# Kernel optimization log

Measured on AMD Instinct MI355X. Metric: run time of the kernel, lower is better.

Reference implementation:

```python
import jax, jax.numpy as jnp
import numpy as np

H = 16          # num_attention_heads
HD = 64         # attention_head_size
ALPHA = 1.5
BANDWIDTH = 1.0
A_EXP = 0.5     # sinkhorn-like exponent 'a'
DIST_SCALE = float(HD)  # alpha < 2 => scale by head_size
EPS = 1e-12     # F.normalize eps


def setup_inputs() -> dict:
    key = jax.random.key(0)
    ks = jax.random.split(key, 5)
    B, L, D = 2, 1024, 1024
    w_scale = 0.02  # keep distances in a non-degenerate range for the power-law kernel
    x = jax.random.normal(ks[0], (B, L, D), dtype=jnp.float32)
    WQ = jax.random.normal(ks[1], (D, D), dtype=jnp.float32) * w_scale
    WK = jax.random.normal(ks[2], (D, D), dtype=jnp.float32) * w_scale
    WV = jax.random.normal(ks[3], (D, D), dtype=jnp.float32) * w_scale
    WO = jax.random.normal(ks[4], (D, D), dtype=jnp.float32) * w_scale
    z = jnp.zeros((D,), dtype=jnp.float32)
    return {"x": x, "WQ": WQ, "bQ": z, "WK": WK, "bK": z,
            "WV": WV, "bV": z, "WO": WO, "bO": z}


def _heads(t, B, L):
    # [B, L, H*HD] -> [B, H, L, HD]
    return t.reshape(B, L, H, HD).transpose(0, 2, 1, 3)


def reference(x, WQ, bQ, WK, bK, WV, bV, WO, bO):
    B, L, D = x.shape
    q = _heads(x @ WQ + bQ, B, L)   # [B,H,L,HD]
    k = _heads(x @ WK + bK, B, L)
    v = _heads(x @ WV + bV, B, L)

    # torch.cdist(q, k, p=2): pairwise euclidean distance [B,H,L,L]
    q2 = jnp.sum(q * q, axis=-1)                      # [B,H,L]
    k2 = jnp.sum(k * k, axis=-1)                      # [B,H,L]
    qk = jnp.einsum('bhid,bhjd->bhij', q, k)          # [B,H,L,L]
    d2 = q2[..., :, None] + k2[..., None, :] - 2.0 * qk
    g_dist = jnp.sqrt(jnp.maximum(d2, EPS)) / DIST_SCALE

    # alpha < 2: power-law kernel (1 + g/sqrt(bw))^(-(d_intrinsic + alpha))
    attn_score = (1.0 + g_dist / np.sqrt(BANDWIDTH)) ** (-(HD + ALPHA))

    # a > 0: Sinkhorn-style row/col renormalization
    N_R = jnp.sum(attn_score, axis=-1)                # [B,H,L] row sums
    N_C = jnp.sum(attn_score, axis=-2)                # [B,H,L] col sums
    K_tilde = (N_R ** (-A_EXP))[..., :, None] * attn_score * (N_C ** (-A_EXP))[..., None, :]

    # F.normalize(p=1, dim=3); entries are positive so |.| sum == sum
    attention_probs = K_tilde / jnp.maximum(jnp.sum(K_tilde, axis=-1, keepdims=True), EPS)

    out = jnp.einsum('bhij,bhjd->bhid', attention_probs, v)   # [B,H,L,HD]
    out = out.transpose(0, 2, 1, 3).reshape(B, L, H * HD)
    return out @ WO + bO
```

## Files before the change

kernel.cpp:

```cpp
#include <hip/hip_runtime.h>
#include <math.h>


typedef __attribute__((ext_vector_type(8))) short short8;
typedef __attribute__((ext_vector_type(4))) float f32x4;

__device__ inline unsigned short f2bf(float f) {
  unsigned int u = __float_as_uint(f);
  unsigned int r = (u + 0x7FFFu + ((u >> 16) & 1u)) >> 16;
  return (unsigned short)r;
}
__device__ inline float bf2f(unsigned short s) {
  return __uint_as_float(((unsigned int)s) << 16);
}
__device__ inline float score_fn(float dot, float sq) {
  float d2 = fmaxf(fmaf(-2.f, dot, sq), 1e-12f);
  float sd = __builtin_amdgcn_sqrtf(d2);
  float lg = __builtin_amdgcn_logf(fmaf(sd, 0.015625f, 1.0f));
  return __builtin_amdgcn_exp2f(-65.5f * lg);
}
__device__ inline unsigned int cvtpk(float lo, float hi) {
  unsigned int r;
  asm("v_cvt_pk_bf16_f32 %0, %1, %2" : "=v"(r) : "v"(lo), "v"(hi));
  return r;
}
#define GLD16(lptr, gptr)                                                      \
  __builtin_amdgcn_global_load_lds(                                            \
      (const __attribute__((address_space(1))) void*)(gptr),                   \
      (__attribute__((address_space(3))) void*)(lptr), 16, 0, 0)
#define MEMFENCE() asm volatile("" ::: "memory")
#define HARD_BARRIER()                 \
  do {                                 \
    __builtin_amdgcn_s_barrier();      \
    MEMFENCE();                        \
  } while (0)

__global__ __launch_bounds__(256) void prep(const float* __restrict__ x,
                                            unsigned short* __restrict__ xb,
                                            const float* __restrict__ W0,
                                            const float* __restrict__ W1,
                                            const float* __restrict__ W2,
                                            const float* __restrict__ W3,
                                            unsigned short* __restrict__ T0,
                                            unsigned short* __restrict__ T1,
                                            unsigned short* __restrict__ T2,
                                            unsigned short* __restrict__ T3) {
  __shared__ float T[32][33];
  int bx = blockIdx.x;
  if (bx < 2048) {
    int i = bx * 256 + threadIdx.x;
    float4 v = ((const float4*)x)[i];
    xb[4 * i + 0] = f2bf(v.x);
    xb[4 * i + 1] = f2bf(v.y);
    xb[4 * i + 2] = f2bf(v.z);
    xb[4 * i + 3] = f2bf(v.w);
    return;
  }
  int idx = bx - 2048;
  int z = idx >> 10, rem = idx & 1023;
  const float* W = z == 0 ? W0 : z == 1 ? W1 : z == 2 ? W2 : W3;
  unsigned short* WT = z == 0 ? T0 : z == 1 ? T1 : z == 2 ? T2 : T3;
  int k0 = (rem >> 5) * 32, n0 = (rem & 31) * 32;
  int c = threadIdx.x & 31, r8 = threadIdx.x >> 5;
#pragma unroll
  for (int it = 0; it < 4; ++it) {
    int rr = r8 + it * 8;
    T[rr][c] = W[(size_t)(k0 + rr) * 1024 + n0 + c];
  }
  __syncthreads();
#pragma unroll
  for (int it = 0; it < 4; ++it) {
    int rr = r8 + it * 8;
    WT[(size_t)(n0 + rr) * 1024 + k0 + c] = f2bf(T[c][rr]);
  }
}

__global__ __launch_bounds__(256, 3) void gemm_qkv(const unsigned short* __restrict__ A,
                                                   const unsigned short* __restrict__ B0,
                                                   const unsigned short* __restrict__ B1,
                                                   const unsigned short* __restrict__ B2,
                                                   const float* __restrict__ c0,
                                                   const float* __restrict__ c1,
                                                   const float* __restrict__ c2,
                                                   void* __restrict__ Y0,
                                                   void* __restrict__ Y1,
                                                   void* __restrict__ Y2,
                                                   float* __restrict__ sq0,
                                                   float* __restrict__ sq1,
                                                   float* __restrict__ sq2,
                                                   int m0, int m1, int m2) {
  int z = blockIdx.z;
  const unsigned short* BT = z == 0 ? B0 : z == 1 ? B1 : B2;
  const float* bias = z == 0 ? c0 : z == 1 ? c1 : c2;
  void* Y = z == 0 ? Y0 : z == 1 ? Y1 : Y2;
  float* sq = z == 0 ? sq0 : z == 1 ? sq1 : sq2;
  int mode = z == 0 ? m0 : z == 1 ? m1 : m2;

  __shared__ __align__(16) unsigned short As[2][128 * 32];
  __shared__ __align__(16) unsigned short Bs[2][64 * 32];
  int tid = threadIdx.x;
  int w = tid >> 6, l = tid & 63, g = l >> 4, l15 = l & 15;
  int wm = w >> 1, wn = w & 1;
  int bm = blockIdx.x * 128, bn = blockIdx.y * 64;

  const int cA0 = tid, cA1 = tid + 256;
  const int rA0 = cA0 >> 2, sA0 = (cA0 & 3) ^ (rA0 & 3) ^ ((rA0 >> 2) & 3);
  const int rA1 = cA1 >> 2, sA1 = (cA1 & 3) ^ (rA1 & 3) ^ ((rA1 >> 2) & 3);
  const int rB0 = tid >> 2, sB0 = (tid & 3) ^ (rB0 & 3) ^ ((rB0 >> 2) & 3);

  GLD16(&As[0][cA0 * 8], &A[(size_t)(bm + rA0) * 1024 + sA0 * 8]);
  GLD16(&As[0][cA1 * 8], &A[(size_t)(bm + rA1) * 1024 + sA1 * 8]);
  GLD16(&Bs[0][tid * 8], &BT[(size_t)(bn + rB0) * 1024 + sB0 * 8]);

  f32x4 acc[4][2];
#pragma unroll
  for (int mi = 0; mi < 4; ++mi)
#pragma unroll
    for (int ni = 0; ni < 2; ++ni)
#pragma unroll
      for (int r = 0; r < 4; ++r) acc[mi][ni][r] = 0.f;

  int arow[4], aslot[4], brow[2], bslot[2];
#pragma unroll
  for (int mi = 0; mi < 4; ++mi) {
    arow[mi] = wm * 64 + mi * 16 + l15;
    aslot[mi] = g ^ (arow[mi] & 3) ^ ((arow[mi] >> 2) & 3);
  }
#pragma unroll
  for (int ni = 0; ni < 2; ++ni) {
    brow[ni] = wn * 32 + ni * 16 + l15;
    bslot[ni] = g ^ (brow[ni] & 3) ^ ((brow[ni] >> 2) & 3);
  }

  __syncthreads();
  for (int t = 0; t < 32; ++t) {
    int cur = t & 1;
    if (t < 31) {
      int kn = (t + 1) * 32;
      GLD16(&As[cur ^ 1][cA0 * 8], &A[(size_t)(bm + rA0) * 1024 + kn + sA0 * 8]);
      GLD16(&As[cur ^ 1][cA1 * 8], &A[(size_t)(bm + rA1) * 1024 + kn + sA1 * 8]);
      GLD16(&Bs[cur ^ 1][tid * 8], &BT[(size_t)(bn + rB0) * 1024 + kn + sB0 * 8]);
    }
    short8 a[4], b[2];
#pragma unroll
    for (int mi = 0; mi < 4; ++mi)
      a[mi] = *(const short8*)&As[cur][arow[mi] * 32 + aslot[mi] * 8];
#pragma unroll
    for (int ni = 0; ni < 2; ++ni)
      b[ni] = *(const short8*)&Bs[cur][brow[ni] * 32 + bslot[ni] * 8];
#pragma unroll
    for (int mi = 0; mi < 4; ++mi)
#pragma unroll
      for (int ni = 0; ni < 2; ++ni)
        acc[mi][ni] = __builtin_amdgcn_mfma_f32_16x16x32_bf16(a[mi], b[ni], acc[mi][ni], 0, 0, 0);
    __syncthreads();
  }

  float rowsq[4][4];
#pragma unroll
  for (int mi = 0; mi < 4; ++mi)
#pragma unroll
    for (int r = 0; r < 4; ++r) rowsq[mi][r] = 0.f;

#pragma unroll
  for (int ni = 0; ni < 2; ++ni) {
    int n = bn + wn * 32 + ni * 16 + l15;
    float bv = bias[n];
#pragma unroll
    for (int mi = 0; mi < 4; ++mi) {
#pragma unroll
      for (int r = 0; r < 4; ++r) {
        int m = bm + wm * 64 + mi * 16 + 4 * g + r;
        float v = acc[mi][ni][r] + bv;
        if (mode == 0) {
          int b = m >> 10, ll = m & 1023, h = n >> 6, hd = n & 63;
          unsigned short ush = f2bf(v);
          ((unsigned short*)Y)[(((size_t)(b * 16 + h) * 1024) + ll) * 64 + hd] = ush;
          float f = bf2f(ush);
          rowsq[mi][r] = fmaf(f, f, rowsq[mi][r]);
        } else if (mode == 1) {
          int b = m >> 10, ll = m & 1023, h = n >> 6, hd = n & 63;
          int jp = (ll & ~31) | (((ll >> 2) & 3) * 8 + ((ll >> 4) & 1) * 4 + (ll & 3));
          ((unsigned short*)Y)[(((size_t)(b * 16 + h) * 64) + hd) * 1024 + jp] = f2bf(v);
        } else {
          ((float*)Y)[(size_t)m * 1024 + n] = v;
        }
      }
    }
  }

  if (sq != nullptr) {
    float* Sq = (float*)&As[0][0];
#pragma unroll
    for (int mi = 0; mi < 4; ++mi)
#pragma unroll
      for (int r = 0; r < 4; ++r) {
        float s = rowsq[mi][r];
        s += __shfl_xor(s, 1);
        s += __shfl_xor(s, 2);
        s += __shfl_xor(s, 4);
        s += __shfl_xor(s, 8);
        rowsq[mi][r] = s;
      }
    if (l15 == 0) {
#pragma unroll
      for (int mi = 0; mi < 4; ++mi)
#pragma unroll
        for (int r = 0; r < 4; ++r)
          Sq[wn * 128 + wm * 64 + mi * 16 + 4 * g + r] = rowsq[mi][r];
    }
    __syncthreads();
    if (tid < 128) {
      float s = Sq[tid] + Sq[128 + tid];
      int m = bm + tid, b = m >> 10, ll = m & 1023;
      int h = bn >> 6;
      sq[(size_t)(b * 16 + h) * 1024 + ll] = s;
    }
  }
}

__global__ __launch_bounds__(256) void gemm_st(const unsigned short* __restrict__ A,
                                               const unsigned short* __restrict__ BT,
                                               const float* __restrict__ bias,
                                               float* __restrict__ Y) {
  __shared__ __align__(16) unsigned short As[2][64 * 64];
  __shared__ __align__(16) unsigned short Bs[2][64 * 64];
  int tid = threadIdx.x;
  int w = tid >> 6, l = tid & 63, g = l >> 4, l15 = l & 15;
  int bm = blockIdx.x * 64, bn = blockIdx.y * 64;
  const int arow = w * 16 + l15;
  const int x7 = l15 & 7;

  const int i0s = tid, i1s = 256 + tid;
  const int r0 = i0s >> 3, s0 = (i0s & 7) ^ (r0 & 7);
  const int r1 = i1s >> 3, s1 = (i1s & 7) ^ (r1 & 7);

  GLD16(&As[0][i0s * 8], &A[(size_t)(bm + r0) * 1024 + s0 * 8]);
  GLD16(&As[0][i1s * 8], &A[(size_t)(bm + r1) * 1024 + s1 * 8]);
  GLD16(&Bs[0][i0s * 8], &BT[(size_t)(bn + r0) * 1024 + s0 * 8]);
  GLD16(&Bs[0][i1s * 8], &BT[(size_t)(bn + r1) * 1024 + s1 * 8]);

  f32x4 acc[4];
#pragma unroll
  for (int t = 0; t < 4; ++t)
#pragma unroll
    for (int r = 0; r < 4; ++r) acc[t][r] = 0.f;

  __syncthreads();
  for (int t = 0; t < 16; ++t) {
    int cur = t & 1;
    if (t < 15) {
      int kn = (t + 1) * 64;
      GLD16(&As[cur ^ 1][i0s * 8], &A[(size_t)(bm + r0) * 1024 + kn + s0 * 8]);
      GLD16(&As[cur ^ 1][i1s * 8], &A[(size_t)(bm + r1) * 1024 + kn + s1 * 8]);
      GLD16(&Bs[cur ^ 1][i0s * 8], &BT[(size_t)(bn + r0) * 1024 + kn + s0 * 8]);
      GLD16(&Bs[cur ^ 1][i1s * 8], &BT[(size_t)(bn + r1) * 1024 + kn + s1 * 8]);
    }
#pragma unroll
    for (int kc = 0; kc < 2; ++kc) {
      short8 a = *(const short8*)&As[cur][arow * 64 + ((kc * 4 + g) ^ x7) * 8];
#pragma unroll
      for (int tt = 0; tt < 4; ++tt) {
        short8 b = *(const short8*)&Bs[cur][(tt * 16 + l15) * 64 + ((kc * 4 + g) ^ x7) * 8];
        acc[tt] = __builtin_amdgcn_mfma_f32_16x16x32_bf16(a, b, acc[tt], 0, 0, 0);
      }
    }
    __syncthreads();
  }

#pragma unroll
  for (int t = 0; t < 4; ++t) {
    int n = bn + 16 * t + l15;
    float bv = bias[n];
#pragma unroll
    for (int r = 0; r < 4; ++r) {
      int m = bm + w * 16 + 4 * g + r;
      Y[(size_t)m * 1024 + n] = acc[t][r] + bv;
    }
  }
}

__global__ __launch_bounds__(256, 4) void colsum_mfma(const unsigned short* __restrict__ Qb,
                                                      const unsigned short* __restrict__ Kb,
                                                      const float* __restrict__ q2,
                                                      const float* __restrict__ k2,
                                                      float* __restrict__ rnc) {
  __shared__ __align__(16) unsigned short Qd[3][64 * 64];
  __shared__ __align__(16) float q2s[1024];
  int bh = blockIdx.x, jt = blockIdx.y;
  int tid = threadIdx.x, w = tid >> 6, l = tid & 63;
  int g = l >> 4, l15 = l & 15;
  const int x7 = l15 & 7;
  const unsigned short* Qp = Qb + (size_t)bh * 65536;
  const unsigned short* Kp = Kb + (size_t)bh * 65536;
  int j = jt * 64 + w * 16 + l15;

  const int i0s = tid, i1s = 256 + tid;
  const int r0 = i0s >> 3, s0 = (i0s & 7) ^ (r0 & 7);
  const int r1 = i1s >> 3, s1 = (i1s & 7) ^ (r1 & 7);

  GLD16(&q2s[tid * 4], q2 + (size_t)bh * 1024 + tid * 4);
  GLD16(&Qd[0][i0s * 8], Qp + (size_t)r0 * 64 + s0 * 8);
  GLD16(&Qd[0][i1s * 8], Qp + (size_t)r1 * 64 + s1 * 8);
  GLD16(&Qd[1][i0s * 8], Qp + (size_t)(64 + r0) * 64 + s0 * 8);
  GLD16(&Qd[1][i1s * 8], Qp + (size_t)(64 + r1) * 64 + s1 * 8);

  short8 bk0 = *(const short8*)&Kp[(size_t)j * 64 + 8 * g];
  short8 bk1 = *(const short8*)&Kp[(size_t)j * 64 + 32 + 8 * g];
  float k2j = k2[(size_t)bh * 1024 + j];
  float colacc = 0.f;

  asm volatile("s_waitcnt vmcnt(2)" ::: "memory");
  HARD_BARRIER();

  for (int t = 0; t < 16; ++t) {
    int cur = t % 3;
    if (t < 14) {
      int nb = (t + 2) % 3;
      int inx = (t + 2) * 64;
      GLD16(&Qd[nb][i0s * 8], Qp + (size_t)(inx + r0) * 64 + s0 * 8);
      GLD16(&Qd[nb][i1s * 8], Qp + (size_t)(inx + r1) * 64 + s1 * 8);
    }
    MEMFENCE();
    const unsigned short* Ql = &Qd[cur][0];
#pragma unroll
    for (int tp = 0; tp < 4; ++tp) {
      int rowb = (16 * tp + l15) * 64;
      short8 a0 = *(const short8*)&Ql[rowb + ((g) ^ x7) * 8];
      short8 a1 = *(const short8*)&Ql[rowb + ((4 + g) ^ x7) * 8];
      f32x4 cf;
#pragma unroll
      for (int r = 0; r < 4; ++r) cf[r] = 0.f;
      __builtin_amdgcn_s_setprio(1);
      cf = __builtin_amdgcn_mfma_f32_16x16x32_bf16(a0, bk0, cf, 0, 0, 0);
      cf = __builtin_amdgcn_mfma_f32_16x16x32_bf16(a1, bk1, cf, 0, 0, 0);
      __builtin_amdgcn_s_setprio(0);
      float4 qv = *(const float4*)&q2s[t * 64 + 16 * tp + 4 * g];
      colacc += score_fn(cf[0], qv.x + k2j);
      colacc += score_fn(cf[1], qv.y + k2j);
      colacc += score_fn(cf[2], qv.z + k2j);
      colacc += score_fn(cf[3], qv.w + k2j);
    }
    if (t < 14) {
      asm volatile("s_waitcnt vmcnt(2)" ::: "memory");
    } else {
      asm volatile("s_waitcnt vmcnt(0)" ::: "memory");
    }
    HARD_BARRIER();
  }
  colacc += __shfl_xor(colacc, 16);
  colacc += __shfl_xor(colacc, 32);
  if (l < 16) rnc[(size_t)bh * 1024 + jt * 64 + w * 16 + l] = __builtin_amdgcn_rsqf(colacc);
}

__global__ __launch_bounds__(256, 2) void attn_mfma(const unsigned short* __restrict__ Qb,
                                                    const unsigned short* __restrict__ Kb,
                                                    const unsigned short* __restrict__ VTp,
                                                    const float* __restrict__ q2,
                                                    const float* __restrict__ k2,
                                                    const float* __restrict__ rnc,
                                                    unsigned short* __restrict__ AO) {
  __shared__ __align__(16) unsigned short Kd[3][64 * 64];
  __shared__ __align__(16) unsigned short Vd[3][64 * 64];
  __shared__ __align__(16) float k2s[1024];
  __shared__ __align__(16) float rns[1024];
  int bh = blockIdx.x;
  int tid = threadIdx.x, w = tid >> 6, l = tid & 63;
  int g = l >> 4, l15 = l & 15;
  const int x7 = l15 & 7;
  int it0 = blockIdx.y * 64 + w * 16;
  const unsigned short* Qp = Qb + (size_t)bh * 65536;
  const unsigned short* Kp = Kb + (size_t)bh * 65536;
  const unsigned short* Vp = VTp + (size_t)bh * 65536;
  int b = bh >> 4, h = bh & 15;

  const int i0s = tid, i1s = 256 + tid;
  const int r0 = i0s >> 3, s0 = (i0s & 7) ^ (r0 & 7);
  const int r1 = i1s >> 3, s1 = (i1s & 7) ^ (r1 & 7);

  GLD16(&k2s[tid * 4], k2 + (size_t)bh * 1024 + tid * 4);
  GLD16(&rns[tid * 4], rnc + (size_t)bh * 1024 + tid * 4);
  GLD16(&Kd[0][i0s * 8], Kp + (size_t)r0 * 64 + s0 * 8);
  GLD16(&Kd[0][i1s * 8], Kp + (size_t)r1 * 64 + s1 * 8);
  GLD16(&Vd[0][i0s * 8], Vp + (size_t)r0 * 1024 + s0 * 8);
  GLD16(&Vd[0][i1s * 8], Vp + (size_t)r1 * 1024 + s1 * 8);
  GLD16(&Kd[1][i0s * 8], Kp + (size_t)(64 + r0) * 64 + s0 * 8);
  GLD16(&Kd[1][i1s * 8], Kp + (size_t)(64 + r1) * 64 + s1 * 8);
  GLD16(&Vd[1][i0s * 8], Vp + (size_t)r0 * 1024 + 64 + s0 * 8);
  GLD16(&Vd[1][i1s * 8], Vp + (size_t)r1 * 1024 + 64 + s1 * 8);

  short8 bq0 = *(const short8*)&Qp[(size_t)(it0 + l15) * 64 + 8 * g];
  short8 bq1 = *(const short8*)&Qp[(size_t)(it0 + l15) * 64 + 32 + 8 * g];
  float q2l = q2[(size_t)bh * 1024 + it0 + l15];

  f32x4 o[4];
#pragma unroll
  for (int t = 0; t < 4; ++t)
#pragma unroll
    for (int r = 0; r < 4; ++r) o[t][r] = 0.f;
  float dacc = 0.f;

  asm volatile("s_waitcnt vmcnt(4)" ::: "memory");
  HARD_BARRIER();

  for (int t = 0; t < 16; ++t) {
    int cur = t % 3;
    if (t < 14) {
      int nb = (t + 2) % 3;
      int j0n = (t + 2) * 64;
      GLD16(&Kd[nb][i0s * 8], Kp + (size_t)(j0n + r0) * 64 + s0 * 8);
      GLD16(&Kd[nb][i1s * 8], Kp + (size_t)(j0n + r1) * 64 + s1 * 8);
      GLD16(&Vd[nb][i0s * 8], Vp + (size_t)r0 * 1024 + j0n + s0 * 8);
      GLD16(&Vd[nb][i1s * 8], Vp + (size_t)r1 * 1024 + j0n + s1 * 8);
    }
    MEMFENCE();
    const unsigned short* Kl = &Kd[cur][0];
    const unsigned short* Vl = &Vd[cur][0];
    int j0 = t * 64;
    float sc[16];
#pragma unroll
    for (int tp = 0; tp < 4; ++tp) {
      int rowb = (16 * tp + l15) * 64;
      short8 a0 = *(const short8*)&Kl[rowb + ((g) ^ x7) * 8];
      short8 a1 = *(const short8*)&Kl[rowb + ((4 + g) ^ x7) * 8];
      f32x4 cf;
#pragma unroll
      for (int r = 0; r < 4; ++r) cf[r] = 0.f;
      __builtin_amdgcn_s_setprio(1);
      cf = __builtin_amdgcn_mfma_f32_16x16x32_bf16(a0, bq0, cf, 0, 0, 0);
      cf = __builtin_amdgcn_mfma_f32_16x16x32_bf16(a1, bq1, cf, 0, 0, 0);
      __builtin_amdgcn_s_setprio(0);
      float4 kv = *(const float4*)&k2s[j0 + 16 * tp + 4 * g];
      float4 rv = *(const float4*)&rns[j0 + 16 * tp + 4 * g];
      sc[tp * 4 + 0] = score_fn(cf[0], q2l + kv.x) * rv.x;
      sc[tp * 4 + 1] = score_fn(cf[1], q2l + kv.y) * rv.y;
      sc[tp * 4 + 2] = score_fn(cf[2], q2l + kv.z) * rv.z;
      sc[tp * 4 + 3] = score_fn(cf[3], q2l + kv.w) * rv.w;
    }
#pragma unroll
    for (int i = 0; i < 16; ++i) dacc += sc[i];
    int pi0[4], pi1[4];
    pi0[0] = (int)cvtpk(sc[0], sc[1]);
    pi0[1] = (int)cvtpk(sc[2], sc[3]);
    pi0[2] = (int)cvtpk(sc[4], sc[5]);
    pi0[3] = (int)cvtpk(sc[6], sc[7]);
    pi1[0] = (int)cvtpk(sc[8], sc[9]);
    pi1[1] = (int)cvtpk(sc[10], sc[11]);
    pi1[2] = (int)cvtpk(sc[12], sc[13]);
    pi1[3] = (int)cvtpk(sc[14], sc[15]);
    short8 pa0 = *(short8*)pi0;
    short8 pa1 = *(short8*)pi1;
#pragma unroll
    for (int t5 = 0; t5 < 4; ++t5) {
      int rowb = (16 * t5 + l15) * 64;
      short8 v0 = *(const short8*)&Vl[rowb + ((g) ^ x7) * 8];
      short8 v1 = *(const short8*)&Vl[rowb + ((4 + g) ^ x7) * 8];
      __builtin_amdgcn_s_setprio(1);
      o[t5] = __builtin_amdgcn_mfma_f32_16x16x32_bf16(pa0, v0, o[t5], 0, 0, 0);
      o[t5] = __builtin_amdgcn_mfma_f32_16x16x32_bf16(pa1, v1, o[t5], 0, 0, 0);
      __builtin_amdgcn_s_setprio(0);
    }
    if (t < 14) {
      asm volatile("s_waitcnt vmcnt(4)" ::: "memory");
    } else {
      asm volatile("s_waitcnt vmcnt(0)" ::: "memory");
    }
    HARD_BARRIER();
  }

  dacc += __shfl_xor(dacc, 16);
  dacc += __shfl_xor(dacc, 32);
  float dv[4];
#pragma unroll
  for (int r = 0; r < 4; ++r) dv[r] = __shfl(dacc, 4 * g + r);

#pragma unroll
  for (int t = 0; t < 4; ++t) {
#pragma unroll
    for (int r = 0; r < 4; ++r) {
      int m = b * 1024 + it0 + 4 * g + r;
      int n = h * 64 + t * 16 + l15;
      AO[(size_t)m * 1024 + n] = f2bf(o[t][r] / dv[r]);
    }
  }
}

extern "C" void kernel_launch(void* const* d_in, const int* in_sizes, int n_in,
                              void* d_out, int out_size, void* d_ws, size_t ws_size,
                              hipStream_t stream) {
  const float* x  = (const float*)d_in[0];
  const float* WQ = (const float*)d_in[1];
  const float* bQ = (const float*)d_in[2];
  const float* WK = (const float*)d_in[3];
  const float* bK = (const float*)d_in[4];
  const float* WV = (const float*)d_in[5];
  const float* bV = (const float*)d_in[6];
  const float* WO = (const float*)d_in[7];
  const float* bO = (const float*)d_in[8];

  char* base = (char*)d_ws;
  unsigned short* xb  = (unsigned short*)(base);
  unsigned short* WQT = (unsigned short*)(base + (4u  << 20));
  unsigned short* WKT = (unsigned short*)(base + (6u  << 20));
  unsigned short* WVT = (unsigned short*)(base + (8u  << 20));
  unsigned short* WOT = (unsigned short*)(base + (10u << 20));
  unsigned short* Qb  = (unsigned short*)(base + (12u << 20));
  unsigned short* Kb  = (unsigned short*)(base + (16u << 20));
  unsigned short* VTp = (unsigned short*)(base + (20u << 20));
  unsigned short* AOb = (unsigned short*)(base + (24u << 20));
  float* q2  = (float*)(base + (28u << 20));
  float* k2  = (float*)(base + (28u << 20) + (128u << 10));
  float* rnc = (float*)(base + (28u << 20) + (256u << 10));

  prep<<<6144, 256, 0, stream>>>(x, xb, WQ, WK, WV, WO, WQT, WKT, WVT, WOT);

  gemm_qkv<<<dim3(16, 16, 3), 256, 0, stream>>>(xb, WQT, WKT, WVT, bQ, bK, bV,
                                                Qb, Kb, VTp, q2, k2, nullptr,
                                                0, 0, 1);

  colsum_mfma<<<dim3(32, 16), 256, 0, stream>>>(Qb, Kb, q2, k2, rnc);
  attn_mfma<<<dim3(32, 16), 256, 0, stream>>>(Qb, Kb, VTp, q2, k2, rnc, AOb);

  gemm_st<<<dim3(32, 16), 256, 0, stream>>>(AOb, WOT, bO, (float*)d_out);
}
```

Before: 97.53 us.

## Fuse colsum, attention and output projection into one cooperative kernel

Replaces three separate kernel launches (column-sum, attention, output GEMM) with one cooperative persistent kernel of 512 blocks that runs each phase in turn, separated by grid-wide syncs and reusing a single shared-memory buffer. This removes two kernel launch gaps and the associated tail effects. In exchange it adds grid.sync cost, requires all 512 blocks to be co-resident (2 per CU with the larger shared buffer), and fixes the occupancy of every phase to the attention phase's launch bounds.

New measurement: 209.3 us. +114.6%, slower.

```diff
diff --git a/kernel.cpp b/kernel.cpp
--- a/kernel.cpp
+++ b/kernel.cpp
@@ -1,5 +1,8 @@
 #include <hip/hip_runtime.h>
+#include <hip/hip_cooperative_groups.h>
 #include <math.h>
+
+namespace cg = cooperative_groups;
 
 
 typedef __attribute__((ext_vector_type(8))) short short8;
@@ -219,268 +222,262 @@
   }
 }
 
-__global__ __launch_bounds__(256) void gemm_st(const unsigned short* __restrict__ A,
-                                               const unsigned short* __restrict__ BT,
-                                               const float* __restrict__ bias,
-                                               float* __restrict__ Y) {
-  __shared__ __align__(16) unsigned short As[2][64 * 64];
-  __shared__ __align__(16) unsigned short Bs[2][64 * 64];
-  int tid = threadIdx.x;
-  int w = tid >> 6, l = tid & 63, g = l >> 4, l15 = l & 15;
-  int bm = blockIdx.x * 64, bn = blockIdx.y * 64;
-  const int arow = w * 16 + l15;
+__global__ __launch_bounds__(256, 2) void fused_tail(const unsigned short* __restrict__ Qb,
+                                                     const unsigned short* __restrict__ Kb,
+                                                     const unsigned short* __restrict__ VTp,
+                                                     const float* __restrict__ q2,
+                                                     const float* __restrict__ k2,
+                                                     float* __restrict__ rnc,
+                                                     unsigned short* __restrict__ AOb,
+                                                     const unsigned short* __restrict__ WOT,
+                                                     const float* __restrict__ bO,
+                                                     float* __restrict__ out) {
+  __shared__ __align__(16) char smem[57344];
+  cg::grid_group grid = cg::this_grid();
+  int blk = blockIdx.x;
+  int tid = threadIdx.x, w = tid >> 6, l = tid & 63;
+  int g = l >> 4, l15 = l & 15;
   const int x7 = l15 & 7;
-
   const int i0s = tid, i1s = 256 + tid;
   const int r0 = i0s >> 3, s0 = (i0s & 7) ^ (r0 & 7);
   const int r1 = i1s >> 3, s1 = (i1s & 7) ^ (r1 & 7);
-
-  GLD16(&As[0][i0s * 8], &A[(size_t)(bm + r0) * 1024 + s0 * 8]);
-  GLD16(&As[0][i1s * 8], &A[(size_t)(bm + r1) * 1024 + s1 * 8]);
-  GLD16(&Bs[0][i0s * 8], &BT[(size_t)(bn + r0) * 1024 + s0 * 8]);
-  GLD16(&Bs[0][i1s * 8], &BT[(size_t)(bn + r1) * 1024 + s1 * 8]);
-
-  f32x4 acc[4];
-#pragma unroll
-  for (int t = 0; t < 4; ++t)
-#pragma unroll
-    for (int r = 0; r < 4; ++r) acc[t][r] = 0.f;
-
-  __syncthreads();
-  for (int t = 0; t < 16; ++t) {
-    int cur = t & 1;
-    if (t < 15) {
-      int kn = (t + 1) * 64;
-      GLD16(&As[cur ^ 1][i0s * 8], &A[(size_t)(bm + r0) * 1024 + kn + s0 * 8]);
-      GLD16(&As[cur ^ 1][i1s * 8], &A[(size_t)(bm + r1) * 1024 + kn + s1 * 8]);
-      GLD16(&Bs[cur ^ 1][i0s * 8], &BT[(size_t)(bn + r0) * 1024 + kn + s0 * 8]);
-      GLD16(&Bs[cur ^ 1][i1s * 8], &BT[(size_t)(bn + r1) * 1024 + kn + s1 * 8]);
-    }
-#pragma unroll
-    for (int kc = 0; kc < 2; ++kc) {
-      short8 a = *(const short8*)&As[cur][arow * 64 + ((kc * 4 + g) ^ x7) * 8];
-#pragma unroll
-      for (int tt = 0; tt < 4; ++tt) {
-        short8 b = *(const short8*)&Bs[cur][(tt * 16 + l15) * 64 + ((kc * 4 + g) ^ x7) * 8];
-        acc[tt] = __builtin_amdgcn_mfma_f32_16x16x32_bf16(a, b, acc[tt], 0, 0, 0);
-      }
-    }
-    __syncthreads();
-  }
-
-#pragma unroll
-  for (int t = 0; t < 4; ++t) {
-    int n = bn + 16 * t + l15;
-    float bv = bias[n];
-#pragma unroll
-    for (int r = 0; r < 4; ++r) {
-      int m = bm + w * 16 + 4 * g + r;
-      Y[(size_t)m * 1024 + n] = acc[t][r] + bv;
-    }
-  }
-}
-
-__global__ __launch_bounds__(256, 4) void colsum_mfma(const unsigned short* __restrict__ Qb,
-                                                      const unsigned short* __restrict__ Kb,
-                                                      const float* __restrict__ q2,
-                                                      const float* __restrict__ k2,
-                                                      float* __restrict__ rnc) {
-  __shared__ __align__(16) unsigned short Qd[3][64 * 64];
-  __shared__ __align__(16) float q2s[1024];
-  int bh = blockIdx.x, jt = blockIdx.y;
-  int tid = threadIdx.x, w = tid >> 6, l = tid & 63;
-  int g = l >> 4, l15 = l & 15;
-  const int x7 = l15 & 7;
-  const unsigned short* Qp = Qb + (size_t)bh * 65536;
-  const unsigned short* Kp = Kb + (size_t)bh * 65536;
-  int j = jt * 64 + w * 16 + l15;
-
-  const int i0s = tid, i1s = 256 + tid;
-  const int r0 = i0s >> 3, s0 = (i0s & 7) ^ (r0 & 7);
-  const int r1 = i1s >> 3, s1 = (i1s & 7) ^ (r1 & 7);
-
-  GLD16(&q2s[tid * 4], q2 + (size_t)bh * 1024 + tid * 4);
-  GLD16(&Qd[0][i0s * 8], Qp + (size_t)r0 * 64 + s0 * 8);
-  GLD16(&Qd[0][i1s * 8], Qp + (size_t)r1 * 64 + s1 * 8);
-  GLD16(&Qd[1][i0s * 8], Qp + (size_t)(64 + r0) * 64 + s0 * 8);
-  GLD16(&Qd[1][i1s * 8], Qp + (size_t)(64 + r1) * 64 + s1 * 8);
-
-  short8 bk0 = *(const short8*)&Kp[(size_t)j * 64 + 8 * g];
-  short8 bk1 = *(const short8*)&Kp[(size_t)j * 64 + 32 + 8 * g];
-  float k2j = k2[(size_t)bh * 1024 + j];
-  float colacc = 0.f;
-
-  asm volatile("s_waitcnt vmcnt(2)" ::: "memory");
-  HARD_BARRIER();
-
-  for (int t = 0; t < 16; ++t) {
-    int cur = t % 3;
-    if (t < 14) {
-      int nb = (t + 2) % 3;
-      int inx = (t + 2) * 64;
-      GLD16(&Qd[nb][i0s * 8], Qp + (size_t)(inx + r0) * 64 + s0 * 8);
-      GLD16(&Qd[nb][i1s * 8], Qp + (size_t)(inx + r1) * 64 + s1 * 8);
-    }
-    MEMFENCE();
-    const unsigned short* Ql = &Qd[cur][0];
-#pragma unroll
-    for (int tp = 0; tp < 4; ++tp) {
-      int rowb = (16 * tp + l15) * 64;
-      short8 a0 = *(const short8*)&Ql[rowb + ((g) ^ x7) * 8];
-      short8 a1 = *(const short8*)&Ql[rowb + ((4 + g) ^ x7) * 8];
-      f32x4 cf;
-#pragma unroll
-      for (int r = 0; r < 4; ++r) cf[r] = 0.f;
-      __builtin_amdgcn_s_setprio(1);
-      cf = __builtin_amdgcn_mfma_f32_16x16x32_bf16(a0, bk0, cf, 0, 0, 0);
-      cf = __builtin_amdgcn_mfma_f32_16x16x32_bf16(a1, bk1, cf, 0, 0, 0);
-      __builtin_amdgcn_s_setprio(0);
-      float4 qv = *(const float4*)&q2s[t * 64 + 16 * tp + 4 * g];
-      colacc += score_fn(cf[0], qv.x + k2j);
-      colacc += score_fn(cf[1], qv.y + k2j);
-      colacc += score_fn(cf[2], qv.z + k2j);
-      colacc += score_fn(cf[3], qv.w + k2j);
-    }
-    if (t < 14) {
-      asm volatile("s_waitcnt vmcnt(2)" ::: "memory");
-    } else {
+  const int bh = blk >> 4, tile = blk & 15;
+
+  {
+    unsigned short* Qd = (unsigned short*)smem;
+    float* q2s = (float*)(smem + 24576);
+    const unsigned short* Qp = Qb + (size_t)bh * 65536;
+    const unsigned short* Kp = Kb + (size_t)bh * 65536;
+    int j = tile * 64 + w * 16 + l15;
+
+    GLD16(&q2s[tid * 4], q2 + (size_t)bh * 1024 + tid * 4);
+    GLD16(&Qd[0 * 4096 + i0s * 8], Qp + (size_t)r0 * 64 + s0 * 8);
+    GLD16(&Qd[0 * 4096 + i1s * 8], Qp + (size_t)r1 * 64 + s1 * 8);
+    GLD16(&Qd[1 * 4096 + i0s * 8], Qp + (size_t)(64 + r0) * 64 + s0 * 8);
+    GLD16(&Qd[1 * 4096 + i1s * 8], Qp + (size_t)(64 + r1) * 64 + s1 * 8);
+
+    short8 bk0 = *(const short8*)&Kp[(size_t)j * 64 + 8 * g];
+    short8 bk1 = *(const short8*)&Kp[(size_t)j * 64 + 32 + 8 * g];
+    float k2j = k2[(size_t)bh * 1024 + j];
+    float colacc = 0.f;
+
+    asm volatile("s_waitcnt vmcnt(2)" ::: "memory");
+    HARD_BARRIER();
+
+    for (int t = 0; t < 16; ++t) {
+      int cur = t % 3;
+      if (t < 14) {
+        int nb = (t + 2) % 3;
+        int inx = (t + 2) * 64;
+        GLD16(&Qd[nb * 4096 + i0s * 8], Qp + (size_t)(inx + r0) * 64 + s0 * 8);
+        GLD16(&Qd[nb * 4096 + i1s * 8], Qp + (size_t)(inx + r1) * 64 + s1 * 8);
+      }
+      MEMFENCE();
+      const unsigned short* Ql = &Qd[cur * 4096];
+#pragma unroll
+      for (int tp = 0; tp < 4; ++tp) {
+        int rowb = (16 * tp + l15) * 64;
+        short8 a0 = *(const short8*)&Ql[rowb + ((g) ^ x7) * 8];
+        short8 a1 = *(const short8*)&Ql[rowb + ((4 + g) ^ x7) * 8];
+        f32x4 cf;
+#pragma unroll
+        for (int r = 0; r < 4; ++r) cf[r] = 0.f;
+        __builtin_amdgcn_s_setprio(1);
+        cf = __builtin_amdgcn_mfma_f32_16x16x32_bf16(a0, bk0, cf, 0, 0, 0);
+        cf = __builtin_amdgcn_mfma_f32_16x16x32_bf16(a1, bk1, cf, 0, 0, 0);
+        __builtin_amdgcn_s_setprio(0);
+        float4 qv = *(const float4*)&q2s[t * 64 + 16 * tp + 4 * g];
+        colacc += score_fn(cf[0], qv.x + k2j);
+        colacc += score_fn(cf[1], qv.y + k2j);
+        colacc += score_fn(cf[2], qv.z + k2j);
+        colacc += score_fn(cf[3], qv.w + k2j);
+      }
+      if (t < 14) {
+        asm volatile("s_waitcnt vmcnt(2)" ::: "memory");
+      } else {
+        asm volatile("s_waitcnt vmcnt(0)" ::: "memory");
+      }
+      HARD_BARRIER();
+    }
+    colacc += __shfl_xor(colacc, 16);
+    colacc += __shfl_xor(colacc, 32);
+    if (l < 16)
+      rnc[(size_t)bh * 1024 + tile * 64 + w * 16 + l] = __builtin_amdgcn_rsqf(colacc);
+  }
+
+  grid.sync();
+
+  {
+    unsigned short* Kd = (unsigned short*)smem;
+    unsigned short* Vd = (unsigned short*)(smem + 24576);
+    float* k2s = (float*)(smem + 49152);
+    float* rns = (float*)(smem + 53248);
+    int it0 = tile * 64 + w * 16;
+    const unsigned short* Qp = Qb + (size_t)bh * 65536;
+    const unsigned short* Kp = Kb + (size_t)bh * 65536;
+    const unsigned short* Vp = VTp + (size_t)bh * 65536;
+    int b = bh >> 4, h = bh & 15;
+
+    GLD16(&k2s[tid * 4], k2 + (size_t)bh * 1024 + tid * 4);
+    GLD16(&rns[tid * 4], rnc + (size_t)bh * 1024 + tid * 4);
+    GLD16(&Kd[0 * 4096 + i0s * 8], Kp + (size_t)r0 * 64 + s0 * 8);
+    GLD16(&Kd[0 * 4096 + i1s * 8], Kp + (size_t)r1 * 64 + s1 * 8);
+    GLD16(&Vd[0 * 4096 + i0s * 8], Vp + (size_t)r0 * 1024 + s0 * 8);
+    GLD16(&Vd[0 * 4096 + i1s * 8], Vp + (size_t)r1 * 1024 + s1 * 8);
+    GLD16(&Kd[1 * 4096 + i0s * 8], Kp + (size_t)(64 + r0) * 64 + s0 * 8);
+    GLD16(&Kd[1 * 4096 + i1s * 8], Kp + (size_t)(64 + r1) * 64 + s1 * 8);
+    GLD16(&Vd[1 * 4096 + i0s * 8], Vp + (size_t)r0 * 1024 + 64 + s0 * 8);
+    GLD16(&Vd[1 * 4096 + i1s * 8], Vp + (size_t)r1 * 1024 + 64 + s1 * 8);
+
+    short8 bq0 = *(const short8*)&Qp[(size_t)(it0 + l15) * 64 + 8 * g];
+    short8 bq1 = *(const short8*)&Qp[(size_t)(it0 + l15) * 64 + 32 + 8 * g];
+    float q2l = q2[(size_t)bh * 1024 + it0 + l15];
+
+    f32x4 o[4];
+#pragma unroll
+    for (int t = 0; t < 4; ++t)
+#pragma unroll
+      for (int r = 0; r < 4; ++r) o[t][r] = 0.f;
+    float dacc = 0.f;
+
+    asm volatile("s_waitcnt vmcnt(4)" ::: "memory");
+    HARD_BARRIER();
+
+    for (int t = 0; t < 16; ++t) {
+      int cur = t % 3;
+      if (t < 14) {
+        int nb = (t + 2) % 3;
+        int j0n = (t + 2) * 64;
+        GLD16(&Kd[nb * 4096 + i0s * 8], Kp + (size_t)(j0n + r0) * 64 + s0 * 8);
+        GLD16(&Kd[nb * 4096 + i1s * 8], Kp + (size_t)(j0n + r1) * 64 + s1 * 8);
+        GLD16(&Vd[nb * 4096 + i0s * 8], Vp + (size_t)r0 * 1024 + j0n + s0 * 8);
+        GLD16(&Vd[nb * 4096 + i1s * 8], Vp + (size_t)r1 * 1024 + j0n + s1 * 8);
+      }
+      MEMFENCE();
+      const unsigned short* Kl = &Kd[cur * 4096];
+      const unsigned short* Vl = &Vd[cur * 4096];
+      int j0 = t * 64;
+      float sc[16];
+#pragma unroll
+      for (int tp = 0; tp < 4; ++tp) {
+        int rowb = (16 * tp + l15) * 64;
+        short8 a0 = *(const short8*)&Kl[rowb + ((g) ^ x7) * 8];
+        short8 a1 = *(const short8*)&Kl[rowb + ((4 + g) ^ x7) * 8];
+        f32x4 cf;
+#pragma unroll
+        for (int r = 0; r < 4; ++r) cf[r] = 0.f;
+        __builtin_amdgcn_s_setprio(1);
+        cf = __builtin_amdgcn_mfma_f32_16x16x32_bf16(a0, bq0, cf, 0, 0, 0);
+        cf = __builtin_amdgcn_mfma_f32_16x16x32_bf16(a1, bq1, cf, 0, 0, 0);
+        __builtin_amdgcn_s_setprio(0);
+        float4 kv = *(const float4*)&k2s[j0 + 16 * tp + 4 * g];
+        float4 rv = *(const float4*)&rns[j0 + 16 * tp + 4 * g];
+        sc[tp * 4 + 0] = score_fn(cf[0], q2l + kv.x) * rv.x;
+        sc[tp * 4 + 1] = score_fn(cf[1], q2l + kv.y) * rv.y;
+        sc[tp * 4 + 2] = score_fn(cf[2], q2l + kv.z) * rv.z;
+        sc[tp * 4 + 3] = score_fn(cf[3], q2l + kv.w) * rv.w;
+      }
+#pragma unroll
+      for (int i = 0; i < 16; ++i) dacc += sc[i];
+      int pi0[4], pi1[4];
+      pi0[0] = (int)cvtpk(sc[0], sc[1]);
+      pi0[1] = (int)cvtpk(sc[2], sc[3]);
+      pi0[2] = (int)cvtpk(sc[4], sc[5]);
+      pi0[3] = (int)cvtpk(sc[6], sc[7]);
+      pi1[0] = (int)cvtpk(sc[8], sc[9]);
+      pi1[1] = (int)cvtpk(sc[10], sc[11]);
+      pi1[2] = (int)cvtpk(sc[12], sc[13]);
+      pi1[3] = (int)cvtpk(sc[14], sc[15]);
+      short8 pa0 = *(short8*)pi0;
+      short8 pa1 = *(short8*)pi1;
+#pragma unroll
+      for (int t5 = 0; t5 < 4; ++t5) {
+        int rowb = (16 * t5 + l15) * 64;
+        short8 v0 = *(const short8*)&Vl[rowb + ((g) ^ x7) * 8];
+        short8 v1 = *(const short8*)&Vl[rowb + ((4 + g) ^ x7) * 8];
+        __builtin_amdgcn_s_setprio(1);
+        o[t5] = __builtin_amdgcn_mfma_f32_16x16x32_bf16(pa0, v0, o[t5], 0, 0, 0);
+        o[t5] = __builtin_amdgcn_mfma_f32_16x16x32_bf16(pa1, v1, o[t5], 0, 0, 0);
+        __builtin_amdgcn_s_setprio(0);
+      }
+      if (t < 14) {
+        asm volatile("s_waitcnt vmcnt(4)" ::: "memory");
+      } else {
+        asm volatile("s_waitcnt vmcnt(0)" ::: "memory");
+      }
+      HARD_BARRIER();
+    }
+
+    dacc += __shfl_xor(dacc, 16);
+    dacc += __shfl_xor(dacc, 32);
+    float dv[4];
+#pragma unroll
+    for (int r = 0; r < 4; ++r) dv[r] = __shfl(dacc, 4 * g + r);
+
+#pragma unroll
+    for (int t = 0; t < 4; ++t) {
+#pragma unroll
+      for (int r = 0; r < 4; ++r) {
+        int m = b * 1024 + it0 + 4 * g + r;
+        int n = h * 64 + t * 16 + l15;
+        AOb[(size_t)m * 1024 + n] = f2bf(o[t][r] / dv[r]);
+      }
+    }
+  }
+
+  grid.sync();
+
+  {
+    unsigned short* As = (unsigned short*)smem;
+    unsigned short* Bs = (unsigned short*)(smem + 16384);
+    int bm = bh * 64, bn = tile * 64;
+    const int arow = w * 16 + l15;
+
+    GLD16(&As[0 * 4096 + i0s * 8], &AOb[(size_t)(bm + r0) * 1024 + s0 * 8]);
+    GLD16(&As[0 * 4096 + i1s * 8], &AOb[(size_t)(bm + r1) * 1024 + s1 * 8]);
+    GLD16(&Bs[0 * 4096 + i0s * 8], &WOT[(size_t)(bn + r0) * 1024 + s0 * 8]);
+    GLD16(&Bs[0 * 4096 + i1s * 8], &WOT[(size_t)(bn + r1) * 1024 + s1 * 8]);
+
+    f32x4 acc[4];
+#pragma unroll
+    for (int t = 0; t < 4; ++t)
+#pragma unroll
+      for (int r = 0; r < 4; ++r) acc[t][r] = 0.f;
+
+    asm volatile("s_waitcnt vmcnt(0)" ::: "memory");
+    HARD_BARRIER();
+    for (int t = 0; t < 16; ++t) {
+      int cur = t & 1;
+      if (t < 15) {
+        int kn = (t + 1) * 64;
+        GLD16(&As[(cur ^ 1) * 4096 + i0s * 8], &AOb[(size_t)(bm + r0) * 1024 + kn + s0 * 8]);
+        GLD16(&As[(cur ^ 1) * 4096 + i1s * 8], &AOb[(size_t)(bm + r1) * 1024 + kn + s1 * 8]);
+        GLD16(&Bs[(cur ^ 1) * 4096 + i0s * 8], &WOT[(size_t)(bn + r0) * 1024 + kn + s0 * 8]);
+        GLD16(&Bs[(cur ^ 1) * 4096 + i1s * 8], &WOT[(size_t)(bn + r1) * 1024 + kn + s1 * 8]);
+      }
+      MEMFENCE();
+#pragma unroll
+      for (int kc = 0; kc < 2; ++kc) {
+        short8 a = *(const short8*)&As[cur * 4096 + arow * 64 + ((kc * 4 + g) ^ x7) * 8];
+#pragma unroll
+        for (int tt = 0; tt < 4; ++tt) {
+          short8 b = *(const short8*)&Bs[cur * 4096 + (tt * 16 + l15) * 64 + ((kc * 4 + g) ^ x7) * 8];
+          acc[tt] = __builtin_amdgcn_mfma_f32_16x16x32_bf16(a, b, acc[tt], 0, 0, 0);
+        }
+      }
       asm volatile("s_waitcnt vmcnt(0)" ::: "memory");
-    }
-    HARD_BARRIER();
-  }
-  colacc += __shfl_xor(colacc, 16);
-  colacc += __shfl_xor(colacc, 32);
-  if (l < 16) rnc[(size_t)bh * 1024 + jt * 64 + w * 16 + l] = __builtin_amdgcn_rsqf(colacc);
-}
-
-__global__ __launch_bounds__(256, 2) void attn_mfma(const unsigned short* __restrict__ Qb,
-                                                    const unsigned short* __restrict__ Kb,
-                                                    const unsigned short* __restrict__ VTp,
-                                                    const float* __restrict__ q2,
-                                                    const float* __restrict__ k2,
-                                                    const float* __restrict__ rnc,
-                                                    unsigned short* __restrict__ AO) {
-  __shared__ __align__(16) unsigned short Kd[3][64 * 64];
-  __shared__ __align__(16) unsigned short Vd[3][64 * 64];
-  __shared__ __align__(16) float k2s[1024];
-  __shared__ __align__(16) float rns[1024];
-  int bh = blockIdx.x;
-  int tid = threadIdx.x, w = tid >> 6, l = tid & 63;
-  int g = l >> 4, l15 = l & 15;
-  const int x7 = l15 & 7;
-  int it0 = blockIdx.y * 64 + w * 16;
-  const unsigned short* Qp = Qb + (size_t)bh * 65536;
-  const unsigned short* Kp = Kb + (size_t)bh * 65536;
-  const unsigned short* Vp = VTp + (size_t)bh * 65536;
-  int b = bh >> 4, h = bh & 15;
-
-  const int i0s = tid, i1s = 256 + tid;
-  const int r0 = i0s >> 3, s0 = (i0s & 7) ^ (r0 & 7);
-  const int r1 = i1s >> 3, s1 = (i1s & 7) ^ (r1 & 7);
-
-  GLD16(&k2s[tid * 4], k2 + (size_t)bh * 1024 + tid * 4);
-  GLD16(&rns[tid * 4], rnc + (size_t)bh * 1024 + tid * 4);
-  GLD16(&Kd[0][i0s * 8], Kp + (size_t)r0 * 64 + s0 * 8);
-  GLD16(&Kd[0][i1s * 8], Kp + (size_t)r1 * 64 + s1 * 8);
-  GLD16(&Vd[0][i0s * 8], Vp + (size_t)r0 * 1024 + s0 * 8);
-  GLD16(&Vd[0][i1s * 8], Vp + (size_t)r1 * 1024 + s1 * 8);
-  GLD16(&Kd[1][i0s * 8], Kp + (size_t)(64 + r0) * 64 + s0 * 8);
-  GLD16(&Kd[1][i1s * 8], Kp + (size_t)(64 + r1) * 64 + s1 * 8);
-  GLD16(&Vd[1][i0s * 8], Vp + (size_t)r0 * 1024 + 64 + s0 * 8);
-  GLD16(&Vd[1][i1s * 8], Vp + (size_t)r1 * 1024 + 64 + s1 * 8);
-
-  short8 bq0 = *(const short8*)&Qp[(size_t)(it0 + l15) * 64 + 8 * g];
-  short8 bq1 = *(const short8*)&Qp[(size_t)(it0 + l15) * 64 + 32 + 8 * g];
-  float q2l = q2[(size_t)bh * 1024 + it0 + l15];
-
-  f32x4 o[4];
-#pragma unroll
-  for (int t = 0; t < 4; ++t)
-#pragma unroll
-    for (int r = 0; r < 4; ++r) o[t][r] = 0.f;
-  float dacc = 0.f;
-
-  asm volatile("s_waitcnt vmcnt(4)" ::: "memory");
-  HARD_BARRIER();
-
-  for (int t = 0; t < 16; ++t) {
-    int cur = t % 3;
-    if (t < 14) {
-      int nb = (t + 2) % 3;
-      int j0n = (t + 2) * 64;
-      GLD16(&Kd[nb][i0s * 8], Kp + (size_t)(j0n + r0) * 64 + s0 * 8);
-      GLD16(&Kd[nb][i1s * 8], Kp + (size_t)(j0n + r1) * 64 + s1 * 8);
-      GLD16(&Vd[nb][i0s * 8], Vp + (size_t)r0 * 1024 + j0n + s0 * 8);
-      GLD16(&Vd[nb][i1s * 8], Vp + (size_t)r1 * 1024 + j0n + s1 * 8);
-    }
-    MEMFENCE();
-    const unsigned short* Kl = &Kd[cur][0];
-    const unsigned short* Vl = &Vd[cur][0];
-    int j0 = t * 64;
-    float sc[16];
-#pragma unroll
-    for (int tp = 0; tp < 4; ++tp) {
-      int rowb = (16 * tp + l15) * 64;
-      short8 a0 = *(const short8*)&Kl[rowb + ((g) ^ x7) * 8];
-      short8 a1 = *(const short8*)&Kl[rowb + ((4 + g) ^ x7) * 8];
-      f32x4 cf;
-#pragma unroll
-      for (int r = 0; r < 4; ++r) cf[r] = 0.f;
-      __builtin_amdgcn_s_setprio(1);
-      cf = __builtin_amdgcn_mfma_f32_16x16x32_bf16(a0, bq0, cf, 0, 0, 0);
-      cf = __builtin_amdgcn_mfma_f32_16x16x32_bf16(a1, bq1, cf, 0, 0, 0);
-      __builtin_amdgcn_s_setprio(0);
-      float4 kv = *(const float4*)&k2s[j0 + 16 * tp + 4 * g];
-      float4 rv = *(const float4*)&rns[j0 + 16 * tp + 4 * g];
-      sc[tp * 4 + 0] = score_fn(cf[0], q2l + kv.x) * rv.x;
-      sc[tp * 4 + 1] = score_fn(cf[1], q2l + kv.y) * rv.y;
-      sc[tp * 4 + 2] = score_fn(cf[2], q2l + kv.z) * rv.z;
-      sc[tp * 4 + 3] = score_fn(cf[3], q2l + kv.w) * rv.w;
-    }
-#pragma unroll
-    for (int i = 0; i < 16; ++i) dacc += sc[i];
-    int pi0[4], pi1[4];
-    pi0[0] = (int)cvtpk(sc[0], sc[1]);
-    pi0[1] = (int)cvtpk(sc[2], sc[3]);
-    pi0[2] = (int)cvtpk(sc[4], sc[5]);
-    pi0[3] = (int)cvtpk(sc[6], sc[7]);
-    pi1[0] = (int)cvtpk(sc[8], sc[9]);
-    pi1[1] = (int)cvtpk(sc[10], sc[11]);
-    pi1[2] = (int)cvtpk(sc[12], sc[13]);
-    pi1[3] = (int)cvtpk(sc[14], sc[15]);
-    short8 pa0 = *(short8*)pi0;
-    short8 pa1 = *(short8*)pi1;
-#pragma unroll
-    for (int t5 = 0; t5 < 4; ++t5) {
-      int rowb = (16 * t5 + l15) * 64;
-      short8 v0 = *(const short8*)&Vl[rowb + ((g) ^ x7) * 8];
-      short8 v1 = *(const short8*)&Vl[rowb + ((4 + g) ^ x7) * 8];
-      __builtin_amdgcn_s_setprio(1);
-      o[t5] = __builtin_amdgcn_mfma_f32_16x16x32_bf16(pa0, v0, o[t5], 0, 0, 0);
-      o[t5] = __builtin_amdgcn_mfma_f32_16x16x32_bf16(pa1, v1, o[t5], 0, 0, 0);
-      __builtin_amdgcn_s_setprio(0);
-    }
-    if (t < 14) {
-      asm volatile("s_waitcnt vmcnt(4)" ::: "memory");
-    } else {
-      asm volatile("s_waitcnt vmcnt(0)" ::: "memory");
-    }
-    HARD_BARRIER();
-  }
-
-  dacc += __shfl_xor(dacc, 16);
-  dacc += __shfl_xor(dacc, 32);
-  float dv[4];
-#pragma unroll
-  for (int r = 0; r < 4; ++r) dv[r] = __shfl(dacc, 4 * g + r);
-
-#pragma unroll
-  for (int t = 0; t < 4; ++t) {
-#pragma unroll
-    for (int r = 0; r < 4; ++r) {
-      int m = b * 1024 + it0 + 4 * g + r;
-      int n = h * 64 + t * 16 + l15;
-      AO[(size_t)m * 1024 + n] = f2bf(o[t][r] / dv[r]);
+      HARD_BARRIER();
+    }
+
+#pragma unroll
+    for (int t = 0; t < 4; ++t) {
+      int n = bn + 16 * t + l15;
+      float bv = bO[n];
+#pragma unroll
+      for (int r = 0; r < 4; ++r) {
+        int m = bm + w * 16 + 4 * g + r;
+        out[(size_t)m * 1024 + n] = acc[t][r] + bv;
+      }
     }
   }
 }
@@ -511,6 +508,7 @@
   float* q2  = (float*)(base + (28u << 20));
   float* k2  = (float*)(base + (28u << 20) + (128u << 10));
   float* rnc = (float*)(base + (28u << 20) + (256u << 10));
+  float* outp = (float*)d_out;
 
   prep<<<6144, 256, 0, stream>>>(x, xb, WQ, WK, WV, WO, WQT, WKT, WVT, WOT);
 
@@ -518,8 +516,8 @@
                                                 Qb, Kb, VTp, q2, k2, nullptr,
                                                 0, 0, 1);
 
-  colsum_mfma<<<dim3(32, 16), 256, 0, stream>>>(Qb, Kb, q2, k2, rnc);
-  attn_mfma<<<dim3(32, 16), 256, 0, stream>>>(Qb, Kb, VTp, q2, k2, rnc, AOb);
-
-  gemm_st<<<dim3(32, 16), 256, 0, stream>>>(AOb, WOT, bO, (float*)d_out);
-}
+  void* args[] = {(void*)&Qb, (void*)&Kb, (void*)&VTp, (void*)&q2, (void*)&k2,
+                  (void*)&rnc, (void*)&AOb, (void*)&WOT, (void*)&bO, (void*)&outp};
+  hipLaunchCooperativeKernel((const void*)fused_tail, dim3(512), dim3(256),
+                             args, 0, stream);
+}
```
